# Optimization experiments

Hardware: AMD Instinct MI355X
Metric: run time of the kernel (lower is better)

Reference implementation:

```python
import jax, jax.numpy as jnp
import numpy as np

D_MODEL = 768
N_HEADS = 12
HEAD_DIM = D_MODEL // N_HEADS


def setup_inputs() -> dict:
    key = jax.random.key(0)
    ks = jax.random.split(key, 9)
    B, S = 2, 2048
    x = jax.random.normal(ks[0], (B, S, D_MODEL), dtype=jnp.float32)
    s = 1.0 / np.sqrt(D_MODEL)
    Wq = jax.random.normal(ks[1], (D_MODEL, D_MODEL), dtype=jnp.float32) * s
    bq = jax.random.normal(ks[2], (D_MODEL,), dtype=jnp.float32) * 0.01
    Wk = jax.random.normal(ks[3], (D_MODEL, D_MODEL), dtype=jnp.float32) * s
    bk = jax.random.normal(ks[4], (D_MODEL,), dtype=jnp.float32) * 0.01
    Wv = jax.random.normal(ks[5], (D_MODEL, D_MODEL), dtype=jnp.float32) * s
    bv = jax.random.normal(ks[6], (D_MODEL,), dtype=jnp.float32) * 0.01
    Wo = jax.random.normal(ks[7], (D_MODEL, D_MODEL), dtype=jnp.float32) * s
    bo = jax.random.normal(ks[8], (D_MODEL,), dtype=jnp.float32) * 0.01
    return {"x": x, "Wq": Wq, "bq": bq, "Wk": Wk, "bk": bk,
            "Wv": Wv, "bv": bv, "Wo": Wo, "bo": bo}


def reference(x, Wq, bq, Wk, bk, Wv, bv, Wo, bo):
    B, S, _ = x.shape
    H, Dh = N_HEADS, HEAD_DIM
    # Projections (torch Linear: x @ W.T + b; here W stored as [in, out])
    q = (x @ Wq + bq).reshape(B, S, H, Dh)
    k = (x @ Wk + bk).reshape(B, S, H, Dh)
    v = (x @ Wv + bv).reshape(B, S, H, Dh)
    scale = 1.0 / jnp.sqrt(jnp.float32(Dh))
    # NOTE: source applies no causal mask despite the class name.
    scores = jnp.einsum('bqhd,bkhd->bhqk', q, k) * scale
    attn = jax.nn.softmax(scores, axis=-1)
    out = jnp.einsum('bhqk,bkhd->bqhd', attn, v).reshape(B, S, H * Dh)
    return out @ Wo + bo
```

## Files before the change

kernel.cpp:

```cpp
#include <hip/hip_runtime.h>

typedef unsigned short u16;
typedef __fp16 halfx2 __attribute__((ext_vector_type(2)));
typedef __fp16 halfx8 __attribute__((ext_vector_type(8)));
typedef float floatx4 __attribute__((ext_vector_type(4)));
typedef unsigned short u16x4 __attribute__((ext_vector_type(4)));
typedef unsigned short u16x8 __attribute__((ext_vector_type(8)));

#define D_MODEL 768
#define NH 12
#define DH 64
#define SEQ 2048
#define BATCH 2
#define MTOK 4096
#define DQKV 2304

__device__ __forceinline__ u16 f2h(float f) {
    __fp16 h = (__fp16)f;
    return __builtin_bit_cast(u16, h);
}

__device__ __forceinline__ void gload_lds16(const void* g, void* l) {
    __builtin_amdgcn_global_load_lds(
        (const __attribute__((address_space(1))) void*)g,
        (__attribute__((address_space(3))) void*)l, 16, 0, 0);
}


__global__ __launch_bounds__(256) void wprep_kernel(const float* __restrict__ Wq, const float* __restrict__ Wk,
                                                    const float* __restrict__ Wv, const float* __restrict__ Wo,
                                                    const float* __restrict__ x,
                                                    u16* __restrict__ WqkvT, u16* __restrict__ WoT,
                                                    u16* __restrict__ xh) {
    __shared__ u16 t[64][72];
    int bid = blockIdx.x;
    int tid = threadIdx.x;
    if (bid >= 576) {
        int idx = (bid - 576) * 2048 + tid * 8;
        float4 v0 = *(const float4*)(x + idx);
        float4 v1 = *(const float4*)(x + idx + 4);
        union { u16x8 u; halfx2 h[4]; } pk;
        pk.h[0] = __builtin_amdgcn_cvt_pkrtz(v0.x, v0.y);
        pk.h[1] = __builtin_amdgcn_cvt_pkrtz(v0.z, v0.w);
        pk.h[2] = __builtin_amdgcn_cvt_pkrtz(v1.x, v1.y);
        pk.h[3] = __builtin_amdgcn_cvt_pkrtz(v1.z, v1.w);
        *(u16x8*)(xh + idx) = pk.u;
        return;
    }
    int z = bid / 144;
    int t2 = bid % 144;
    int k0 = (t2 / 12) * 64, n0 = (t2 % 12) * 64;
    const float* W = (z == 0) ? Wq : (z == 1) ? Wk : (z == 2) ? Wv : Wo;
    u16* dst = (z < 3) ? (WqkvT + (size_t)z * 768 * 768) : WoT;
#pragma unroll
    for (int p = 0; p < 16; ++p) {
        int idx = p * 256 + tid;
        int kr = idx >> 6, nc = idx & 63;
        t[kr][nc] = f2h(W[(size_t)(k0 + kr) * 768 + n0 + nc]);
    }
    __syncthreads();
#pragma unroll
    for (int p = 0; p < 16; ++p) {
        int idx = p * 256 + tid;
        int nr = idx >> 6, kc = idx & 63;
        dst[(size_t)(n0 + nr) * 768 + k0 + kc] = t[kc][nr];
    }
}


__global__ __launch_bounds__(256) void gemm_qkv(const u16* __restrict__ xh, const u16* __restrict__ Bt,
                                                const float* __restrict__ bq, const float* __restrict__ bk,
                                                const float* __restrict__ bv,
                                                u16* __restrict__ qP, u16* __restrict__ kP,
                                                u16* __restrict__ vTout) {
    const int tid = threadIdx.x;
    const int wid = tid >> 6;
    const int lane = tid & 63;
    const int qd = lane >> 4;
    const int l15 = lane & 15;

    const int tn = blockIdx.x * 128;
    const int tm = blockIdx.y * 64;
    const int wm = (wid >> 1) * 32;
    const int wn = (wid & 1) * 64;

    __shared__ alignas(16) u16 As[64 * 64];
    __shared__ alignas(16) u16 Bs[128 * 64];

    floatx4 acc[2][4];
#pragma unroll
    for (int i = 0; i < 2; ++i)
#pragma unroll
        for (int j = 0; j < 4; ++j) acc[i][j] = (floatx4)(0.0f);

    const u16* Ag[2];
#pragma unroll
    for (int rd = 0; rd < 2; ++rd) {
        int s = rd * 256 + tid;
        int r = s >> 3, bl = (s & 7) ^ (r & 7);
        Ag[rd] = xh + (size_t)(tm + r) * 768 + bl * 8;
    }
    const u16* Bg[4];
#pragma unroll
    for (int rd = 0; rd < 4; ++rd) {
        int s = rd * 256 + tid;
        int r = s >> 3, bl = (s & 7) ^ (r & 7);
        Bg[rd] = Bt + (size_t)(tn + r) * 768 + bl * 8;
    }

    for (int kb = 0; kb < 768; kb += 64) {
        __syncthreads();
#pragma unroll
        for (int rd = 0; rd < 2; ++rd)
            gload_lds16(Ag[rd] + kb, As + (size_t)(rd * 256 + tid) * 8);
#pragma unroll
        for (int rd = 0; rd < 4; ++rd)
            gload_lds16(Bg[rd] + kb, Bs + (size_t)(rd * 256 + tid) * 8);
        __syncthreads();

#pragma unroll
        for (int ks = 0; ks < 2; ++ks) {
            halfx8 af[2], bf[4];
#pragma unroll
            for (int i = 0; i < 2; ++i) {
                int r = wm + i * 16 + l15;
                af[i] = *(const halfx8*)(As + r * 64 + (((ks * 4 + qd) ^ (r & 7)) * 8));
            }
#pragma unroll
            for (int j = 0; j < 4; ++j) {
                int r2 = wn + j * 16 + l15;
                bf[j] = *(const halfx8*)(Bs + r2 * 64 + (((ks * 4 + qd) ^ (r2 & 7)) * 8));
            }
#pragma unroll
            for (int i = 0; i < 2; ++i)
#pragma unroll
                for (int j = 0; j < 4; ++j)
                    acc[i][j] = __builtin_amdgcn_mfma_f32_16x16x32_f16(af[i], bf[j], acc[i][j], 0, 0, 0);
        }
    }

    const float cscale = 0.125f * 1.44269504088896340736f;
    const int rgn = (tn < 768) ? 0 : (tn < 1536) ? 1 : 2;
    const float* bsrc = (rgn == 0) ? bq : (rgn == 1) ? bk : bv;
#pragma unroll
    for (int j = 0; j < 4; ++j) {
        int col = tn + wn + j * 16 + l15;
        int cl = col - rgn * 768;
        float bvv = bsrc[cl];
        int h = cl >> 6, d = cl & 63;
#pragma unroll
        for (int i = 0; i < 2; ++i) {
            int row0 = tm + wm + i * 16 + qd * 4;
            int b = row0 >> 11, s0 = row0 & 2047;
            u16x4 pk;
#pragma unroll
            for (int r = 0; r < 4; ++r) {
                float v = acc[i][j][r] + bvv;
                if (rgn == 0) v *= cscale;
                pk[r] = f2h(v);
            }
            if (rgn == 2) {
                *(u16x4*)(vTout + ((size_t)(b * NH + h) * 64 + d) * SEQ + s0) = pk;
            } else {
                u16* dst = (rgn == 0) ? qP : kP;
#pragma unroll
                for (int r = 0; r < 4; ++r)
                    dst[((size_t)(b * NH + h) * SEQ + s0 + r) * DH + d] = pk[r];
            }
        }
    }
}


__global__ __launch_bounds__(256, 3) void attn_kernel(const u16* __restrict__ qP, const u16* __restrict__ kP,
                                                      const u16* __restrict__ vT, u16* __restrict__ attn) {
    const int tid = threadIdx.x;
    const int wid = tid >> 6;
    const int lane = tid & 63;
    const int qd = lane >> 4;
    const int l15 = lane & 15;

    const int bh = blockIdx.x;
    const int b = bh / NH, h = bh % NH;
    const int q0 = blockIdx.y * 64;

    __shared__ alignas(16) u16 smem[2 * 64 * 136];

    halfx8 aq[4][2];
#pragma unroll
    for (int jn = 0; jn < 4; ++jn)
#pragma unroll
        for (int ks = 0; ks < 2; ++ks)
            aq[jn][ks] = *(const halfx8*)(qP + (size_t)(bh * SEQ + q0 + jn * 16 + l15) * DH + ks * 32 + qd * 8);

    floatx4 o[4];
#pragma unroll
    for (int jn = 0; jn < 4; ++jn) o[jn] = (floatx4)(0.0f);
    float lsum[4] = {0.0f, 0.0f, 0.0f, 0.0f};

    const u16* kbase = kP + (size_t)(bh * SEQ + wid * 32 + l15) * DH + qd * 8;
    const u16* vbase = vT + (size_t)(bh * 64 + wid * 16 + l15) * SEQ + qd * 8;

    floatx4 sc[2][4];
    {
        halfx8 ak0[2][2];
#pragma unroll
        for (int mi = 0; mi < 2; ++mi)
#pragma unroll
            for (int ks = 0; ks < 2; ++ks)
                ak0[mi][ks] = *(const halfx8*)(kbase + (size_t)(mi * 16) * DH + ks * 32);
#pragma unroll
        for (int jn = 0; jn < 4; ++jn) {
#pragma unroll
            for (int mi = 0; mi < 2; ++mi) {
                floatx4 z = (floatx4)(0.0f);
                z = __builtin_amdgcn_mfma_f32_16x16x32_f16(ak0[mi][0], aq[jn][0], z, 0, 0, 0);
                sc[mi][jn] = __builtin_amdgcn_mfma_f32_16x16x32_f16(ak0[mi][1], aq[jn][1], z, 0, 0, 0);
            }
        }
    }

    for (int kt = 0; kt < 16; ++kt) {
        u16* pbuf = smem + (size_t)(kt & 1) * (64 * 136);
        const int kt1 = (kt + 1) & 15;

        halfx8 akn[2][2];
#pragma unroll
        for (int mi = 0; mi < 2; ++mi)
#pragma unroll
            for (int ks = 0; ks < 2; ++ks)
                akn[mi][ks] = *(const halfx8*)(kbase + (size_t)(kt1 * 128 + mi * 16) * DH + ks * 32);
        halfx8 avc[4];
#pragma unroll
        for (int ks = 0; ks < 4; ++ks)
            avc[ks] = *(const halfx8*)(vbase + kt * 128 + ks * 32);

#pragma unroll
        for (int mi = 0; mi < 2; ++mi)
#pragma unroll
            for (int jn = 0; jn < 4; ++jn) {
                float p0 = __builtin_amdgcn_exp2f(sc[mi][jn][0]);
                float p1 = __builtin_amdgcn_exp2f(sc[mi][jn][1]);
                float p2 = __builtin_amdgcn_exp2f(sc[mi][jn][2]);
                float p3 = __builtin_amdgcn_exp2f(sc[mi][jn][3]);
                lsum[jn] += (p0 + p1) + (p2 + p3);
                union { u16x4 u; halfx2 h[2]; } pk;
                pk.h[0] = __builtin_amdgcn_cvt_pkrtz(p0, p1);
                pk.h[1] = __builtin_amdgcn_cvt_pkrtz(p2, p3);
                *(u16x4*)(pbuf + (jn * 16 + l15) * 136 + wid * 32 + mi * 16 + qd * 4) = pk.u;
            }

        __builtin_amdgcn_s_setprio(1);
#pragma unroll
        for (int jn = 0; jn < 4; ++jn) {
#pragma unroll
            for (int mi = 0; mi < 2; ++mi) {
                floatx4 z = (floatx4)(0.0f);
                z = __builtin_amdgcn_mfma_f32_16x16x32_f16(akn[mi][0], aq[jn][0], z, 0, 0, 0);
                sc[mi][jn] = __builtin_amdgcn_mfma_f32_16x16x32_f16(akn[mi][1], aq[jn][1], z, 0, 0, 0);
            }
        }
        __builtin_amdgcn_s_setprio(0);

        __syncthreads();

        __builtin_amdgcn_s_setprio(1);
#pragma unroll
        for (int ks = 0; ks < 4; ++ks) {
#pragma unroll
            for (int jn = 0; jn < 4; ++jn) {
                halfx8 bp = *(const halfx8*)(pbuf + (jn * 16 + l15) * 136 + ks * 32 + qd * 8);
                o[jn] = __builtin_amdgcn_mfma_f32_16x16x32_f16(avc[ks], bp, o[jn], 0, 0, 0);
            }
        }
        __builtin_amdgcn_s_setprio(0);
    }

#pragma unroll
    for (int jn = 0; jn < 4; ++jn) {
        float v = lsum[jn];
        v += __shfl_xor(v, 16, 64);
        v += __shfl_xor(v, 32, 64);
        lsum[jn] = v;
    }

    float* la4 = (float*)smem;
    if (qd == 0) {
#pragma unroll
        for (int jn = 0; jn < 4; ++jn)
            la4[wid * 64 + jn * 16 + l15] = lsum[jn];
    }
    __syncthreads();

#pragma unroll
    for (int jn = 0; jn < 4; ++jn) {
        int q = jn * 16 + l15;
        float s = (la4[q] + la4[64 + q]) + (la4[128 + q] + la4[192 + q]);
        float inv = __builtin_amdgcn_rcpf(s);
        u16x4 pk;
#pragma unroll
        for (int r = 0; r < 4; ++r) pk[r] = f2h(o[jn][r] * inv);
        u16* dst = attn + (size_t)(b * SEQ + q0 + q) * D_MODEL + h * DH + wid * 16 + qd * 4;
        *(u16x4*)dst = pk;
    }
}


__global__ __launch_bounds__(256) void gemm_out(const u16* __restrict__ A, const u16* __restrict__ Bt,
                                                const float* __restrict__ bias, float* __restrict__ Cout) {
    const int tid = threadIdx.x;
    const int wid = tid >> 6;
    const int lane = tid & 63;
    const int qd = lane >> 4;
    const int l15 = lane & 15;

    const int tn = blockIdx.x * 64;
    const int tm = blockIdx.y * 64;
    const int wm = (wid >> 1) * 32;
    const int wn = (wid & 1) * 32;

    __shared__ alignas(16) u16 As[64 * 64];
    __shared__ alignas(16) u16 Bs[64 * 64];

    floatx4 acc[2][2];
#pragma unroll
    for (int i = 0; i < 2; ++i)
#pragma unroll
        for (int j = 0; j < 2; ++j) acc[i][j] = (floatx4)(0.0f);

    const u16* Ag[2];
    const u16* Bg[2];
#pragma unroll
    for (int rd = 0; rd < 2; ++rd) {
        int s = rd * 256 + tid;
        int r = s >> 3, bl = (s & 7) ^ (r & 7);
        Ag[rd] = A + (size_t)(tm + r) * 768 + bl * 8;
        Bg[rd] = Bt + (size_t)(tn + r) * 768 + bl * 8;
    }

    for (int kb = 0; kb < 768; kb += 64) {
        __syncthreads();
#pragma unroll
        for (int rd = 0; rd < 2; ++rd) {
            gload_lds16(Ag[rd] + kb, As + (size_t)(rd * 256 + tid) * 8);
            gload_lds16(Bg[rd] + kb, Bs + (size_t)(rd * 256 + tid) * 8);
        }
        __syncthreads();

#pragma unroll
        for (int ks = 0; ks < 2; ++ks) {
            halfx8 af[2], bf[2];
#pragma unroll
            for (int i = 0; i < 2; ++i) {
                int r = wm + i * 16 + l15;
                af[i] = *(const halfx8*)(As + r * 64 + (((ks * 4 + qd) ^ (r & 7)) * 8));
                int r2 = wn + i * 16 + l15;
                bf[i] = *(const halfx8*)(Bs + r2 * 64 + (((ks * 4 + qd) ^ (r2 & 7)) * 8));
            }
#pragma unroll
            for (int i = 0; i < 2; ++i)
#pragma unroll
                for (int j = 0; j < 2; ++j)
                    acc[i][j] = __builtin_amdgcn_mfma_f32_16x16x32_f16(af[i], bf[j], acc[i][j], 0, 0, 0);
        }
    }

#pragma unroll
    for (int j = 0; j < 2; ++j) {
        int col = tn + wn + j * 16 + l15;
        float bv = bias[col];
#pragma unroll
        for (int i = 0; i < 2; ++i) {
            int row0 = tm + wm + i * 16 + qd * 4;
#pragma unroll
            for (int r = 0; r < 4; ++r)
                Cout[(size_t)(row0 + r) * 768 + col] = acc[i][j][r] + bv;
        }
    }
}


extern "C" void kernel_launch(void* const* d_in, const int* in_sizes, int n_in,
                              void* d_out, int out_size, void* d_ws, size_t ws_size,
                              hipStream_t stream) {
    const float* x  = (const float*)d_in[0];
    const float* Wq = (const float*)d_in[1];
    const float* bq = (const float*)d_in[2];
    const float* Wk = (const float*)d_in[3];
    const float* bk = (const float*)d_in[4];
    const float* Wv = (const float*)d_in[5];
    const float* bv = (const float*)d_in[6];
    const float* Wo = (const float*)d_in[7];
    const float* bo = (const float*)d_in[8];

    char* ws = (char*)d_ws;
    size_t off = 0;
    auto take = [&](size_t bytes) -> char* {
        char* p = ws + off;
        off += (bytes + 255) & ~(size_t)255;
        return p;
    };
    u16* WqkvT = (u16*)take((size_t)DQKV * D_MODEL * 2);
    u16* WoT   = (u16*)take((size_t)D_MODEL * D_MODEL * 2);
    u16* qP    = (u16*)take((size_t)MTOK * D_MODEL * 2);
    u16* kP    = (u16*)take((size_t)MTOK * D_MODEL * 2);
    u16* vTb   = (u16*)take((size_t)BATCH * NH * DH * SEQ * 2);
    u16* attn  = (u16*)take((size_t)MTOK * D_MODEL * 2);
    u16* xh = attn;

    wprep_kernel<<<576 + (MTOK * D_MODEL / 2048), 256, 0, stream>>>(Wq, Wk, Wv, Wo, x, WqkvT, WoT, xh);
    gemm_qkv<<<dim3(DQKV / 128, MTOK / 64), 256, 0, stream>>>(xh, WqkvT, bq, bk, bv, qP, kP, vTb);
    attn_kernel<<<dim3(BATCH * NH, SEQ / 64), 256, 0, stream>>>(qP, kP, vTb, attn);
    gemm_out<<<dim3(D_MODEL / 64, MTOK / 64), 256, 0, stream>>>(attn, WoT, bo, (float*)d_out);
}
```

Baseline: 185.2 us.

## Split PV work across waves by head-dim and key halves with swizzled P buffer

Each wave now computes a 32-column slice of the head dimension over half of the keys in each tile, instead of a 16-column slice over all keys. Every P fragment read from LDS therefore feeds two MFMAs, which halves LDS read traffic. The padded P layout is replaced by an XOR-swizzled, unpadded layout to avoid bank conflicts. The cost is an extra barrier and a cross-wave LDS reduction of the partial outputs at the end, done through a stride-33 float buffer whose 16-byte vector accesses may be misaligned.

Measured after the change: 179.5 us. -3.1%, faster.

```diff
diff --git a/kernel.cpp b/kernel.cpp
--- a/kernel.cpp
+++ b/kernel.cpp
@@ -179,12 +179,14 @@
     const int lane = tid & 63;
     const int qd = lane >> 4;
     const int l15 = lane & 15;
+    const int r7 = l15 & 7;
+    const int dh = wid >> 1, kh = wid & 1;
 
     const int bh = blockIdx.x;
     const int b = bh / NH, h = bh % NH;
     const int q0 = blockIdx.y * 64;
 
-    __shared__ alignas(16) u16 smem[2 * 64 * 136];
+    __shared__ alignas(16) u16 smem[2 * 64 * 128];
 
     halfx8 aq[4][2];
 #pragma unroll
@@ -193,13 +195,15 @@
         for (int ks = 0; ks < 2; ++ks)
             aq[jn][ks] = *(const halfx8*)(qP + (size_t)(bh * SEQ + q0 + jn * 16 + l15) * DH + ks * 32 + qd * 8);
 
-    floatx4 o[4];
-#pragma unroll
-    for (int jn = 0; jn < 4; ++jn) o[jn] = (floatx4)(0.0f);
+    floatx4 o[2][4];
+#pragma unroll
+    for (int ip = 0; ip < 2; ++ip)
+#pragma unroll
+        for (int jn = 0; jn < 4; ++jn) o[ip][jn] = (floatx4)(0.0f);
     float lsum[4] = {0.0f, 0.0f, 0.0f, 0.0f};
 
     const u16* kbase = kP + (size_t)(bh * SEQ + wid * 32 + l15) * DH + qd * 8;
-    const u16* vbase = vT + (size_t)(bh * 64 + wid * 16 + l15) * SEQ + qd * 8;
+    const u16* vbase = vT + (size_t)(bh * 64 + dh * 32 + l15) * SEQ + kh * 64 + qd * 8;
 
     floatx4 sc[2][4];
     {
@@ -221,7 +225,7 @@
     }
 
     for (int kt = 0; kt < 16; ++kt) {
-        u16* pbuf = smem + (size_t)(kt & 1) * (64 * 136);
+        u16* pbuf = smem + (size_t)(kt & 1) * (64 * 128);
         const int kt1 = (kt + 1) & 15;
 
         halfx8 akn[2][2];
@@ -230,10 +234,12 @@
 #pragma unroll
             for (int ks = 0; ks < 2; ++ks)
                 akn[mi][ks] = *(const halfx8*)(kbase + (size_t)(kt1 * 128 + mi * 16) * DH + ks * 32);
-        halfx8 avc[4];
-#pragma unroll
-        for (int ks = 0; ks < 4; ++ks)
-            avc[ks] = *(const halfx8*)(vbase + kt * 128 + ks * 32);
+        halfx8 avc[2][2];
+#pragma unroll
+        for (int ip = 0; ip < 2; ++ip)
+#pragma unroll
+            for (int ks = 0; ks < 2; ++ks)
+                avc[ip][ks] = *(const halfx8*)(vbase + (size_t)(ip * 16) * SEQ + kt * 128 + ks * 32);
 
 #pragma unroll
         for (int mi = 0; mi < 2; ++mi)
@@ -247,7 +253,8 @@
                 union { u16x4 u; halfx2 h[2]; } pk;
                 pk.h[0] = __builtin_amdgcn_cvt_pkrtz(p0, p1);
                 pk.h[1] = __builtin_amdgcn_cvt_pkrtz(p2, p3);
-                *(u16x4*)(pbuf + (jn * 16 + l15) * 136 + wid * 32 + mi * 16 + qd * 4) = pk.u;
+                *(u16x4*)(pbuf + (jn * 16 + l15) * 128 +
+                          ((wid * 4 + mi * 2 + (qd >> 1)) ^ r7) * 8 + (qd & 1) * 4) = pk.u;
             }
 
         __builtin_amdgcn_s_setprio(1);
@@ -266,11 +273,14 @@
 
         __builtin_amdgcn_s_setprio(1);
 #pragma unroll
-        for (int ks = 0; ks < 4; ++ks) {
+        for (int ks = 0; ks < 2; ++ks) {
 #pragma unroll
             for (int jn = 0; jn < 4; ++jn) {
-                halfx8 bp = *(const halfx8*)(pbuf + (jn * 16 + l15) * 136 + ks * 32 + qd * 8);
-                o[jn] = __builtin_amdgcn_mfma_f32_16x16x32_f16(avc[ks], bp, o[jn], 0, 0, 0);
+                halfx8 bp = *(const halfx8*)(pbuf + (jn * 16 + l15) * 128 +
+                                             ((kh * 8 + ks * 4 + qd) ^ r7) * 8);
+#pragma unroll
+                for (int ip = 0; ip < 2; ++ip)
+                    o[ip][jn] = __builtin_amdgcn_mfma_f32_16x16x32_f16(avc[ip][ks], bp, o[ip][jn], 0, 0, 0);
             }
         }
         __builtin_amdgcn_s_setprio(0);
@@ -284,7 +294,18 @@
         lsum[jn] = v;
     }
 
-    float* la4 = (float*)smem;
+    __syncthreads();
+
+    float* obuf = (float*)smem;
+    float* la4  = (float*)smem + 4352;
+
+    if (kh == 1) {
+#pragma unroll
+        for (int jn = 0; jn < 4; ++jn)
+#pragma unroll
+            for (int ip = 0; ip < 2; ++ip)
+                *(floatx4*)(obuf + (size_t)(dh * 64 + jn * 16 + l15) * 33 + ip * 16 + qd * 4) = o[ip][jn];
+    }
     if (qd == 0) {
 #pragma unroll
         for (int jn = 0; jn < 4; ++jn)
@@ -292,16 +313,21 @@
     }
     __syncthreads();
 
-#pragma unroll
-    for (int jn = 0; jn < 4; ++jn) {
-        int q = jn * 16 + l15;
-        float s = (la4[q] + la4[64 + q]) + (la4[128 + q] + la4[192 + q]);
-        float inv = __builtin_amdgcn_rcpf(s);
-        u16x4 pk;
-#pragma unroll
-        for (int r = 0; r < 4; ++r) pk[r] = f2h(o[jn][r] * inv);
-        u16* dst = attn + (size_t)(b * SEQ + q0 + q) * D_MODEL + h * DH + wid * 16 + qd * 4;
-        *(u16x4*)dst = pk;
+    if (kh == 0) {
+#pragma unroll
+        for (int jn = 0; jn < 4; ++jn) {
+            int q = jn * 16 + l15;
+            float s = (la4[q] + la4[64 + q]) + (la4[128 + q] + la4[192 + q]);
+            float inv = __builtin_amdgcn_rcpf(s);
+#pragma unroll
+            for (int ip = 0; ip < 2; ++ip) {
+                floatx4 val = o[ip][jn] + *(const floatx4*)(obuf + (size_t)(dh * 64 + q) * 33 + ip * 16 + qd * 4);
+                u16x4 pk;
+#pragma unroll
+                for (int r = 0; r < 4; ++r) pk[r] = f2h(val[r] * inv);
+                *(u16x4*)(attn + (size_t)(b * SEQ + q0 + q) * D_MODEL + h * DH + dh * 32 + ip * 16 + qd * 4) = pk;
+            }
+        }
     }
 }
 
```
